# Kernel optimization log

Measured on AMD Instinct MI355X. Metric: run time of the kernel, lower is better.

Reference implementation:

```python
import jax, jax.numpy as jnp
import numpy as np

B, C, H, W = 32, 256, 64, 64
R = 16  # reduction
TOPK = 128


def setup_inputs() -> dict:
    key = jax.random.key(0)
    k_x, k_w1, k_b1, k_w2, k_b2 = jax.random.split(key, 5)
    return {
        "x": jax.random.normal(k_x, (B, C, H, W), dtype=jnp.float32),
        "w1": jax.random.normal(k_w1, (C // R, C), dtype=jnp.float32) * 0.05,
        "b1": jax.random.normal(k_b1, (C // R,), dtype=jnp.float32) * 0.05,
        "w2": jax.random.normal(k_w2, (C, C // R), dtype=jnp.float32) * 0.05,
        "b2": jax.random.normal(k_b2, (C,), dtype=jnp.float32) * 0.05,
        "topk": TOPK,
    }


def reference(x, w1, b1, w2, b2, topk):
    # Global average pool: [B, C, H, W] -> [B, C]
    y = jnp.mean(x, axis=(2, 3))
    # 1x1-conv squeeze-excite MLP (1x1 convs on a 1x1 spatial map == dense layers)
    h = jax.nn.relu(jnp.einsum("bc,rc->br", y, w1) + b1)
    attn_weight = jax.nn.sigmoid(jnp.einsum("br,cr->bc", h, w2) + b2)  # [B, C]
    # top-k channels by attention weight, then sort indices ascending
    _, idx = jax.lax.top_k(attn_weight, topk)          # [B, topk]
    idx = jnp.sort(idx, axis=1)
    # Fused: gather the selected channel weights and channels of x, multiply once
    aw_sel = jnp.take_along_axis(attn_weight, idx, axis=1)        # [B, topk]
    x_sel = jnp.take_along_axis(x, idx[:, :, None, None], axis=1)  # [B, topk, H, W]
    return aw_sel[:, :, None, None] * x_sel
```

## Files before the change

### kernel.cpp

```cpp
#include <hip/hip_runtime.h>

#define NB 32
#define NC 256
#define HW 4096
#define RDIM 16
#define KTOP 128

typedef float v4f __attribute__((ext_vector_type(4)));

__global__ __launch_bounds__(256) void pool_kernel(const float* __restrict__ x,
                                                   float* __restrict__ y) {
    const int wid  = threadIdx.x >> 6;
    const int lane = threadIdx.x & 63;
    const int plane = blockIdx.x * 4 + wid;
    const v4f* __restrict__ xin = (const v4f*)(x + (size_t)plane * HW);
    float s = 0.f;
#pragma unroll
    for (int i = 0; i < 16; ++i) {
        v4f v = xin[lane + i * 64];
        s += (v.x + v.y) + (v.z + v.w);
    }
#pragma unroll
    for (int off = 32; off > 0; off >>= 1) s += __shfl_down(s, off);
    if (lane == 0) y[plane] = s * (1.0f / HW);
}

__global__ __launch_bounds__(256) void se_topk_kernel(
    const float* __restrict__ y,
    const float* __restrict__ w1, const float* __restrict__ b1,
    const float* __restrict__ w2, const float* __restrict__ b2,
    int* __restrict__ idx_out, float* __restrict__ aw_out) {
    const int b = blockIdx.x;
    const int t = threadIdx.x;
    const int wid = t >> 6, lane = t & 63;
    __shared__ float ych[NC];
    __shared__ float hsh[RDIM];
    __shared__ float attn[NC];
    __shared__ unsigned long long masks[4];

    ych[t] = y[b * NC + t];
    __syncthreads();

    const int r = t >> 4;
    const int j = t & 15;
    float partial = 0.f;
#pragma unroll
    for (int k = 0; k < 16; ++k) {
        const int c = j * 16 + k;
        partial += ych[c] * w1[r * NC + c];
    }
#pragma unroll
    for (int m = 8; m > 0; m >>= 1) partial += __shfl_xor(partial, m, 16);
    if (j == 0) hsh[r] = fmaxf(partial + b1[r], 0.f);
    __syncthreads();

    float z = b2[t];
#pragma unroll
    for (int rr = 0; rr < RDIM; ++rr) z += hsh[rr] * w2[t * RDIM + rr];
    const float v = 1.0f / (1.0f + __expf(-z));
    attn[t] = v;
    __syncthreads();

    int rank = 0;
#pragma unroll 4
    for (int c = 0; c < NC; ++c) {
        const float o = attn[c];
        rank += (o > v) || (o == v && c < t);
    }
    const bool s = (rank < KTOP);

    const unsigned long long m = __ballot(s);
    if (lane == 0) masks[wid] = m;
    __syncthreads();
    if (s) {
        int pos = __popcll(m & ((lane == 63) ? 0x7FFFFFFFFFFFFFFFull
                                             : ((1ull << lane) - 1ull)));
        for (int w = 0; w < 4; ++w) pos += (w < wid) ? __popcll(masks[w]) : 0;
        idx_out[b * KTOP + pos] = t;
        aw_out[b * KTOP + pos] = v;
    }
}

__global__ __launch_bounds__(256) void gather_scale_kernel(
    const float* __restrict__ x,
    const int* __restrict__ idx, const float* __restrict__ aw,
    float* __restrict__ out) {
    const int wid  = threadIdx.x >> 6;
    const int lane = threadIdx.x & 63;
    const int p = blockIdx.x * 4 + wid;
    const int b = p >> 7;
    const int c = idx[p];
    const float w = aw[p];
    const v4f* __restrict__ xin =
        (const v4f*)(x + ((size_t)b * NC + c) * HW);
    v4f* __restrict__ o = (v4f*)(out + (size_t)p * HW);
#pragma unroll
    for (int i = 0; i < 16; ++i) {
        v4f v = xin[lane + i * 64];
        v4f rr = v * w;
        __builtin_nontemporal_store(rr, &o[lane + i * 64]);
    }
}

extern "C" void kernel_launch(void* const* d_in, const int* in_sizes, int n_in,
                              void* d_out, int out_size, void* d_ws, size_t ws_size,
                              hipStream_t stream) {
    const float* x  = (const float*)d_in[0];
    const float* w1 = (const float*)d_in[1];
    const float* b1 = (const float*)d_in[2];
    const float* w2 = (const float*)d_in[3];
    const float* b2 = (const float*)d_in[4];
    float* out = (float*)d_out;

    float* y   = (float*)d_ws;
    int*   idx = (int*)(y + NB * NC);
    float* aw  = (float*)(idx + NB * KTOP);

    pool_kernel<<<NB * NC / 4, 256, 0, stream>>>(x, y);
    se_topk_kernel<<<NB, 256, 0, stream>>>(y, w1, b1, w2, b2, idx, aw);
    gather_scale_kernel<<<NB * KTOP / 4, 256, 0, stream>>>(x, idx, aw, out);
}
```

Baseline: 55.10 us.

## Fuse SE MLP and top-k selection into gather kernel, recomputing per block

Merges the SE/top-k kernel with the gather-scale kernel. Each of the 1024 gather blocks now recomputes the MLP, sigmoid and top-k ranking for its batch and keeps the selected indices in shared memory. This drops one kernel launch and the global round trip for idx/aw. In exchange it repeats the small SE computation 32 times per batch, which adds a serial prologue before each block can start its memory-bound copy.

```diff
diff --git a/kernel.cpp b/kernel.cpp
--- a/kernel.cpp
+++ b/kernel.cpp
@@ -25,18 +25,22 @@
     if (lane == 0) y[plane] = s * (1.0f / HW);
 }
 
-__global__ __launch_bounds__(256) void se_topk_kernel(
-    const float* __restrict__ y,
+__global__ __launch_bounds__(256) void se_topk_gather_kernel(
+    const float* __restrict__ x, const float* __restrict__ y,
     const float* __restrict__ w1, const float* __restrict__ b1,
     const float* __restrict__ w2, const float* __restrict__ b2,
-    int* __restrict__ idx_out, float* __restrict__ aw_out) {
-    const int b = blockIdx.x;
-    const int t = threadIdx.x;
+    float* __restrict__ out) {
+    const int blk = blockIdx.x;
+    const int b   = blk >> 5;
+    const int t   = threadIdx.x;
     const int wid = t >> 6, lane = t & 63;
+
     __shared__ float ych[NC];
     __shared__ float hsh[RDIM];
     __shared__ float attn[NC];
     __shared__ unsigned long long masks[4];
+    __shared__ int   sidx[KTOP];
+    __shared__ float saw[KTOP];
 
     ych[t] = y[b * NC + t];
     __syncthreads();
@@ -76,28 +80,20 @@
         int pos = __popcll(m & ((lane == 63) ? 0x7FFFFFFFFFFFFFFFull
                                              : ((1ull << lane) - 1ull)));
         for (int w = 0; w < 4; ++w) pos += (w < wid) ? __popcll(masks[w]) : 0;
-        idx_out[b * KTOP + pos] = t;
-        aw_out[b * KTOP + pos] = v;
+        sidx[pos] = t;
+        saw[pos]  = v;
     }
-}
+    __syncthreads();
 
-__global__ __launch_bounds__(256) void gather_scale_kernel(
-    const float* __restrict__ x,
-    const int* __restrict__ idx, const float* __restrict__ aw,
-    float* __restrict__ out) {
-    const int wid  = threadIdx.x >> 6;
-    const int lane = threadIdx.x & 63;
-    const int p = blockIdx.x * 4 + wid;
-    const int b = p >> 7;
-    const int c = idx[p];
-    const float w = aw[p];
-    const v4f* __restrict__ xin =
-        (const v4f*)(x + ((size_t)b * NC + c) * HW);
-    v4f* __restrict__ o = (v4f*)(out + (size_t)p * HW);
+    const int k = (blk & 31) * 4 + wid;
+    const int c = sidx[k];
+    const float w = saw[k];
+    const v4f* __restrict__ xin = (const v4f*)(x + ((size_t)b * NC + c) * HW);
+    v4f* __restrict__ o = (v4f*)(out + ((size_t)b * KTOP + k) * HW);
 #pragma unroll
     for (int i = 0; i < 16; ++i) {
-        v4f v = xin[lane + i * 64];
-        v4f rr = v * w;
+        v4f vv = xin[lane + i * 64];
+        v4f rr = vv * w;
         __builtin_nontemporal_store(rr, &o[lane + i * 64]);
     }
 }
@@ -112,11 +108,9 @@
     const float* b2 = (const float*)d_in[4];
     float* out = (float*)d_out;
 
-    float* y   = (float*)d_ws;
-    int*   idx = (int*)(y + NB * NC);
-    float* aw  = (float*)(idx + NB * KTOP);
+    float* y = (float*)d_ws;
 
     pool_kernel<<<NB * NC / 4, 256, 0, stream>>>(x, y);
-    se_topk_kernel<<<NB, 256, 0, stream>>>(y, w1, b1, w2, b2, idx, aw);
-    gather_scale_kernel<<<NB * KTOP / 4, 256, 0, stream>>>(x, idx, aw, out);
+    se_topk_gather_kernel<<<NB * KTOP / 4, 256, 0, stream>>>(
+        x, y, w1, b1, w2, b2, out);
 }
```

Measured after the change: 53.79 us. -2.4%, faster.

## Fuse pooling with SE/top-k via last-block-done atomic counter per batch

Applied to the files above, without the earlier changes.

Merges the pooling kernel and the SE-MLP/top-k kernel into one launch. Each block pools four planes, then atomically bumps a per-batch counter, and the last of the 64 blocks for that batch runs the MLP, sigmoid and top-k selection. This drops one kernel launch and the gap between launches, at the cost of a memset launch to zero the counters and a serialized tail where one block per batch does the SE work. A loop unroll factor in the ranking loop also changes.

```diff
diff --git a/kernel.cpp b/kernel.cpp
--- a/kernel.cpp
+++ b/kernel.cpp
@@ -8,31 +8,42 @@
 
 typedef float v4f __attribute__((ext_vector_type(4)));
 
-__global__ __launch_bounds__(256) void pool_kernel(const float* __restrict__ x,
-                                                   float* __restrict__ y) {
-    const int wid  = threadIdx.x >> 6;
-    const int lane = threadIdx.x & 63;
-    const int plane = blockIdx.x * 4 + wid;
-    const v4f* __restrict__ xin = (const v4f*)(x + (size_t)plane * HW);
-    float s = 0.f;
-#pragma unroll
-    for (int i = 0; i < 16; ++i) {
-        v4f v = xin[lane + i * 64];
-        s += (v.x + v.y) + (v.z + v.w);
-    }
-#pragma unroll
-    for (int off = 32; off > 0; off >>= 1) s += __shfl_down(s, off);
-    if (lane == 0) y[plane] = s * (1.0f / HW);
-}
-
-__global__ __launch_bounds__(256) void se_topk_kernel(
-    const float* __restrict__ y,
+__global__ __launch_bounds__(256) void pool_sek_kernel(
+    const float* __restrict__ x, float* __restrict__ y, int* __restrict__ cnt,
     const float* __restrict__ w1, const float* __restrict__ b1,
     const float* __restrict__ w2, const float* __restrict__ b2,
     int* __restrict__ idx_out, float* __restrict__ aw_out) {
-    const int b = blockIdx.x;
-    const int t = threadIdx.x;
+    const int blk = blockIdx.x;
+    const int b   = blk >> 6;
+    const int t   = threadIdx.x;
     const int wid = t >> 6, lane = t & 63;
+
+    const int plane = blk * 4 + wid;
+    {
+        const v4f* __restrict__ xin = (const v4f*)(x + (size_t)plane * HW);
+        float s = 0.f;
+#pragma unroll
+        for (int i = 0; i < 16; ++i) {
+            v4f v = xin[lane + i * 64];
+            s += (v.x + v.y) + (v.z + v.w);
+        }
+#pragma unroll
+        for (int off = 32; off > 0; off >>= 1) s += __shfl_down(s, off);
+        if (lane == 0) y[plane] = s * (1.0f / HW);
+    }
+    __syncthreads();
+
+    __shared__ int amLast;
+    if (t == 0) {
+        const int prev = __hip_atomic_fetch_add(&cnt[b], 1, __ATOMIC_ACQ_REL,
+                                                __HIP_MEMORY_SCOPE_AGENT);
+        amLast = (prev == 63);
+    }
+    __syncthreads();
+    if (!amLast) return;
+
+    __builtin_amdgcn_fence(__ATOMIC_ACQUIRE, "agent");
+
     __shared__ float ych[NC];
     __shared__ float hsh[RDIM];
     __shared__ float attn[NC];
@@ -62,7 +73,7 @@
     __syncthreads();
 
     int rank = 0;
-#pragma unroll 4
+#pragma unroll 8
     for (int c = 0; c < NC; ++c) {
         const float o = attn[c];
         rank += (o > v) || (o == v && c < t);
@@ -77,11 +88,11 @@
                                              : ((1ull << lane) - 1ull)));
         for (int w = 0; w < 4; ++w) pos += (w < wid) ? __popcll(masks[w]) : 0;
         idx_out[b * KTOP + pos] = t;
-        aw_out[b * KTOP + pos] = v;
+        aw_out[b * KTOP + pos]  = v;
     }
 }
 
-__global__ __launch_bounds__(256) void gather_scale_kernel(
+__global__ __launch_bounds__(256) void gather_kernel(
     const float* __restrict__ x,
     const int* __restrict__ idx, const float* __restrict__ aw,
     float* __restrict__ out) {
@@ -91,13 +102,12 @@
     const int b = p >> 7;
     const int c = idx[p];
     const float w = aw[p];
-    const v4f* __restrict__ xin =
-        (const v4f*)(x + ((size_t)b * NC + c) * HW);
+    const v4f* __restrict__ xin = (const v4f*)(x + ((size_t)b * NC + c) * HW);
     v4f* __restrict__ o = (v4f*)(out + (size_t)p * HW);
 #pragma unroll
     for (int i = 0; i < 16; ++i) {
-        v4f v = xin[lane + i * 64];
-        v4f rr = v * w;
+        v4f vv = xin[lane + i * 64];
+        v4f rr = vv * w;
         __builtin_nontemporal_store(rr, &o[lane + i * 64]);
     }
 }
@@ -113,10 +123,13 @@
     float* out = (float*)d_out;
 
     float* y   = (float*)d_ws;
-    int*   idx = (int*)(y + NB * NC);
+    int*   cnt = (int*)(y + NB * NC);
+    int*   idx = cnt + NB;
     float* aw  = (float*)(idx + NB * KTOP);
 
-    pool_kernel<<<NB * NC / 4, 256, 0, stream>>>(x, y);
-    se_topk_kernel<<<NB, 256, 0, stream>>>(y, w1, b1, w2, b2, idx, aw);
-    gather_scale_kernel<<<NB * KTOP / 4, 256, 0, stream>>>(x, idx, aw, out);
+    (void)hipMemsetAsync(cnt, 0, NB * sizeof(int), stream);
+
+    pool_sek_kernel<<<NB * NC / 4, 256, 0, stream>>>(
+        x, y, cnt, w1, b1, w2, b2, idx, aw);
+    gather_kernel<<<NB * KTOP / 4, 256, 0, stream>>>(x, idx, aw, out);
 }
```

Result: slower. 131.4 us (+138.5%).
